# Optimization experiments

Hardware: AMD Instinct MI355X
Metric: run time of the kernel (lower is better)

Reference implementation:

```python
import jax, jax.numpy as jnp
import numpy as np

B, T, D = 2, 4096, 1024
H, L = 8, 2
DH = D // H           # 128
BS = 64               # bucket_size (lucidrains default)
NH = 8                # n_hashes (lucidrains default)
NB = T // BS          # 64 buckets (even, required)
FF = 4 * D


def setup_inputs() -> dict:
    key = jax.random.key(0)
    ks = jax.random.split(key, 16)
    s = 0.02
    return {
        'x': jax.random.normal(ks[0], (B, T, D), jnp.float32),
        'Wqk': jax.random.normal(ks[1], (L, D, H * DH), jnp.float32) * s,
        'Wv': jax.random.normal(ks[2], (L, D, H * DH), jnp.float32) * s,
        'Wout': jax.random.normal(ks[3], (L, H * DH, D), jnp.float32) * s,
        'bout': jnp.zeros((L, D), jnp.float32),
        'ln1_g': jnp.ones((L, D), jnp.float32),
        'ln1_b': jnp.zeros((L, D), jnp.float32),
        'W1': jax.random.normal(ks[4], (L, D, FF), jnp.float32) * s,
        'b1': jnp.zeros((L, FF), jnp.float32),
        'W2': jax.random.normal(ks[5], (L, FF, D), jnp.float32) * s,
        'b2': jnp.zeros((L, D), jnp.float32),
        'ln2_g': jnp.ones((L, D), jnp.float32),
        'ln2_b': jnp.zeros((L, D), jnp.float32),
        'rotations': jax.random.normal(ks[6], (L, DH, NH, NB // 2), jnp.float32),
    }


def _layer_norm(x, g, b):
    m = jnp.mean(x, axis=-1, keepdims=True)
    v = jnp.var(x, axis=-1, keepdims=True)
    return (x - m) * jax.lax.rsqrt(v + 1e-5) * g + b


def _look_one_back(x):
    # concat each chunk with the previous chunk (wrap-around), along the within-chunk axis
    return jnp.concatenate([x, jnp.roll(x, 1, axis=1)], axis=2)


def _lsh_attention(qk, v, rot):
    # qk, v: (bh, T, DH); rot: (DH, NH, NB//2). Causal LSH attention (lucidrains defaults).
    bh, t, d = qk.shape
    rotated = jnp.einsum('btd,dhr->bhtr', qk, rot)
    rotated = jnp.concatenate([rotated, -rotated], axis=-1)          # (bh, NH, T, NB)
    buckets = jnp.argmax(rotated, axis=-1)                            # (bh, NH, T)
    buckets = buckets + (jnp.arange(NH) * NB)[None, :, None]
    buckets = buckets.reshape(bh, NH * t)
    ticker = jnp.arange(NH * t)
    buckets_and_t = buckets * t + (ticker % t)
    sticker = jnp.argsort(buckets_and_t, axis=-1)                     # stable
    undo_sort = jnp.argsort(sticker, axis=-1)
    st = sticker % t                                                  # original positions
    sqk = jnp.take_along_axis(qk, st[..., None], axis=1)              # (bh, NH*T, DH)
    sv = jnp.take_along_axis(v, st[..., None], axis=1)
    n_chunks = NH * NB
    bq = sqk.reshape(bh, n_chunks, BS, d)
    norm = jnp.maximum(jnp.linalg.norm(sqk, axis=-1, keepdims=True), 1e-12)
    bk = (sqk / norm).reshape(bh, n_chunks, BS, d)
    bv = sv.reshape(bh, n_chunks, BS, d)
    bk = _look_one_back(bk)                                           # (bh, nc, 2*BS, d)
    bv = _look_one_back(bv)
    dots = jnp.einsum('bcie,bcje->bcij', bq, bk) * (d ** -0.5)
    bq_t = st.reshape(bh, n_chunks, BS)
    bkv_t = _look_one_back(bq_t[..., None] * jnp.ones((1,), st.dtype))[..., 0] if False else jnp.concatenate([bq_t, jnp.roll(bq_t, 1, axis=1)], axis=2)
    causal = bq_t[:, :, :, None] < bkv_t[:, :, None, :]
    dots = jnp.where(causal, -1e9, dots)
    self_mask = bq_t[:, :, :, None] == bkv_t[:, :, None, :]
    dots = jnp.where(self_mask, -5e4, dots)                           # TOKEN_SELF_ATTN_VALUE
    lse = jax.scipy.special.logsumexp(dots, axis=-1, keepdims=True)
    p = jnp.exp(dots - lse)
    bo = jnp.einsum('bcij,bcje->bcie', p, bv)
    so = bo.reshape(bh, NH * t, d)
    o = jnp.take_along_axis(so, undo_sort[..., None], axis=1)
    logits = jnp.take_along_axis(lse.reshape(bh, NH * t), undo_sort, axis=1)
    o = o.reshape(bh, NH, t, d)
    logits = logits.reshape(bh, NH, t, 1)
    probs = jnp.exp(logits - jax.scipy.special.logsumexp(logits, axis=1, keepdims=True))
    return jnp.sum(o * probs, axis=1)                                 # (bh, T, DH)


def _attn_block(x, Wqk, Wv, Wout, bout, g, b, rot):
    h = _layer_norm(x, g, b)
    qk = (h @ Wqk).reshape(B, T, H, DH).transpose(0, 2, 1, 3).reshape(B * H, T, DH)
    v = (h @ Wv).reshape(B, T, H, DH).transpose(0, 2, 1, 3).reshape(B * H, T, DH)
    o = _lsh_attention(qk, v, rot)
    o = o.reshape(B, H, T, DH).transpose(0, 2, 1, 3).reshape(B, T, H * DH)
    return o @ Wout + bout


def _ff_block(x, W1, b1, W2, b2, g, b):
    h = _layer_norm(x, g, b)
    return jax.nn.gelu(h @ W1 + b1, approximate=False) @ W2 + b2


def reference(x, Wqk, Wv, Wout, bout, ln1_g, ln1_b, W1, b1, W2, b2, ln2_g, ln2_b, rotations):
    # Reversible Reformer: x duplicated into two streams
    x1, x2 = x, x
    for l in range(L):
        x1 = x1 + _attn_block(x2, Wqk[l], Wv[l], Wout[l], bout[l], ln1_g[l], ln1_b[l], rotations[l])
        x2 = x2 + _ff_block(x1, W1[l], b1[l], W2[l], b2[l], ln2_g[l], ln2_b[l])
    out = (x1 + x2) * 0.5
    # mean-pool over sequence, reshape (1, B, D)
    return jnp.mean(out, axis=1).reshape(1, -1, D)
```

## Files before the change

### kernel.cpp

```cpp
#include <hip/hip_runtime.h>
#include <hip/hip_bf16.h>
#include <stdint.h>

#define B_ 2
#define T_ 4096
#define D_ 1024
#define H_ 8
#define DH_ 128
#define L_ 2
#define BS_ 64
#define NH_ 8
#define NB_ 64
#define NC_ (NH_*NB_)
#define FF_ 4096
#define BH_ (B_*H_)

typedef __hip_bfloat16 bf16;
typedef __attribute__((ext_vector_type(8))) short short8;
typedef __attribute__((ext_vector_type(4))) float f32x4;

typedef __attribute__((address_space(3))) uint32_t lds_u32_t;
typedef const __attribute__((address_space(1))) uint32_t glb_u32_t;

__device__ __forceinline__ void async_load16(const void* g, void* l) {
  __builtin_amdgcn_global_load_lds((glb_u32_t*)g, (lds_u32_t*)l, 16, 0, 0);
}

__global__ void diag_kernel(float* __restrict__ out, float a, float b) {
  if (threadIdx.x == 0) { out[0] = a; out[1] = b; }
}

__global__ void copy2_kernel(const float* __restrict__ x, float* __restrict__ x1,
                             float* __restrict__ x2) {
  int idx = blockIdx.x * 256 + threadIdx.x;
  if (idx < B_ * T_ * D_ / 4) {
    float4 v = ((const float4*)x)[idx];
    ((float4*)x1)[idx] = v;
    ((float4*)x2)[idx] = v;
  }
}

__global__ __launch_bounds__(256)
void transpose_cvt(const float* __restrict__ src, bf16* __restrict__ dst, int K, int N) {
  __shared__ float tile[32][33];
  const int n0 = blockIdx.x * 32, k0 = blockIdx.y * 32;
  const int c = threadIdx.x & 31, r8 = threadIdx.x >> 5;
#pragma unroll
  for (int i = 0; i < 32; i += 8) tile[r8 + i][c] = src[(size_t)(k0 + r8 + i) * N + n0 + c];
  __syncthreads();
#pragma unroll
  for (int i = 0; i < 32; i += 8)
    dst[(size_t)(n0 + r8 + i) * K + k0 + c] = __float2bfloat16(tile[c][r8 + i]);
}

__global__ __launch_bounds__(256)
void ln_kernel(const float* __restrict__ x, const float* __restrict__ g,
               const float* __restrict__ b, bf16* __restrict__ h) {
  __shared__ float red[8];
  const int row = blockIdx.x;
  const float* xr = x + (size_t)row * D_;
  const int tid = threadIdx.x;
  float4 xv = *(const float4*)(xr + tid * 4);
  float vals[4] = {xv.x, xv.y, xv.z, xv.w};
  float s = vals[0] + vals[1] + vals[2] + vals[3];
  float s2 = vals[0]*vals[0] + vals[1]*vals[1] + vals[2]*vals[2] + vals[3]*vals[3];
#pragma unroll
  for (int o = 1; o < 64; o <<= 1) { s += __shfl_xor(s, o, 64); s2 += __shfl_xor(s2, o, 64); }
  const int w = tid >> 6, lane = tid & 63;
  if (lane == 0) { red[w] = s; red[4 + w] = s2; }
  __syncthreads();
  s = red[0] + red[1] + red[2] + red[3];
  s2 = red[4] + red[5] + red[6] + red[7];
  const float mean = s * (1.0f / D_);
  const float var = s2 * (1.0f / D_) - mean * mean;
  const float rstd = rsqrtf(var + 1e-5f);
  bf16* hr = h + (size_t)row * D_;
#pragma unroll
  for (int i = 0; i < 4; ++i) {
    const int c = tid * 4 + i;
    hr[c] = __float2bfloat16((vals[i] - mean) * rstd * g[c] + b[c]);
  }
}

template<int EPI>
__global__ __launch_bounds__(512)
void gemm_bt_k(const bf16* __restrict__ A, const bf16* __restrict__ Bt,
               void* __restrict__ dst, const float* __restrict__ bias,
               float* __restrict__ resid, int M, int N, int K) {
  __shared__ __align__(16) bf16 sA[2][128 * 64];
  __shared__ __align__(16) bf16 sB[2][128 * 64];
  const int tid = threadIdx.x;

  const int GX = gridDim.x;
  const int nwg = GX * gridDim.y;
  const int orig = blockIdx.y * GX + blockIdx.x;
  int m0, n0;
  if ((nwg & 7) == 0 && (gridDim.y & 7) == 0) {
    const int cpx = nwg >> 3;
    const int lin = (orig & 7) * cpx + (orig >> 3);
    const int gsz = GX << 3;
    const int group = lin / gsz;
    const int rem = lin - group * gsz;
    m0 = ((group << 3) + (rem & 7)) << 7;
    n0 = (rem >> 3) << 7;
  } else {
    m0 = blockIdx.y << 7;
    n0 = blockIdx.x << 7;
  }

  const int lane = tid & 63;
  const int wv = tid >> 6;
  const int wm = (wv >> 2) << 6;
  const int wn = (wv & 3) << 5;
  const int l15 = lane & 15, lq = lane >> 4;

  f32x4 acc[4][2];
#pragma unroll
  for (int i = 0; i < 4; ++i)
#pragma unroll
    for (int j = 0; j < 2; ++j) acc[i][j] = (f32x4){0.f, 0.f, 0.f, 0.f};

  const bf16* Ab = A + (size_t)m0 * K;
  const bf16* Bb = Bt + (size_t)n0 * K;

  const int r0s = tid >> 3, ch0 = tid & 7;
  const int r1s = r0s + 64;
  const size_t sa0 = (size_t)r0s * K + (size_t)((ch0 ^ (r0s & 7)) << 3);
  const size_t sa1 = (size_t)r1s * K + (size_t)((ch0 ^ (r1s & 7)) << 3);

  auto stage = [&](int t) {
    const int b = t & 1;
    const size_t ko = (size_t)t << 6;
    async_load16(Ab + sa0 + ko, (char*)sA[b] + tid * 16);
    async_load16(Ab + sa1 + ko, (char*)sA[b] + (tid + 512) * 16);
    async_load16(Bb + sa0 + ko, (char*)sB[b] + tid * 16);
    async_load16(Bb + sa1 + ko, (char*)sB[b] + (tid + 512) * 16);
  };

  auto compute = [&](int b) {
    const bf16* __restrict__ pA = sA[b];
    const bf16* __restrict__ pB = sB[b];
#pragma unroll
    for (int kk = 0; kk < 2; ++kk) {
      short8 af[4], bfr[2];
#pragma unroll
      for (int mi = 0; mi < 4; ++mi) {
        const int row = wm + mi * 16 + l15;
        const int chunk = (kk * 4 + lq) ^ (row & 7);
        af[mi] = *(const short8*)(pA + (row << 6) + (chunk << 3));
      }
#pragma unroll
      for (int ni = 0; ni < 2; ++ni) {
        const int row = wn + ni * 16 + l15;
        const int chunk = (kk * 4 + lq) ^ (row & 7);
        bfr[ni] = *(const short8*)(pB + (row << 6) + (chunk << 3));
      }
#pragma unroll
      for (int mi = 0; mi < 4; ++mi)
#pragma unroll
        for (int ni = 0; ni < 2; ++ni)
          acc[mi][ni] = __builtin_amdgcn_mfma_f32_16x16x32_bf16(af[mi], bfr[ni], acc[mi][ni], 0, 0, 0);
    }
  };

  stage(0);
  __syncthreads();
  const int NT = K >> 6;
  for (int t = 0; t < NT; ++t) {
    if (t + 1 < NT) stage(t + 1);
    compute(t & 1);
    if (t + 1 < NT) __syncthreads();
  }

  const int cr = lq << 2;
  if (EPI == 5) {
    const int hh2 = (n0 + wn) >> 5;
#pragma unroll
    for (int mi = 0; mi < 4; ++mi) {
#pragma unroll
      for (int j = 0; j < 4; ++j) {
        const float v0 = acc[mi][0][j], v1 = acc[mi][1][j];
        float bmx = v0; int imx = l15;
        if (v1 > bmx) { bmx = v1; imx = 16 + l15; }
        float bmn = v0; int imn = l15;
        if (v1 < bmn) { bmn = v1; imn = 16 + l15; }
#pragma unroll
        for (int o = 1; o < 16; o <<= 1) {
          const float ov = __shfl_xor(bmx, o, 64); const int oi = __shfl_xor(imx, o, 64);
          if (ov > bmx || (ov == bmx && oi < imx)) { bmx = ov; imx = oi; }
          const float ov2 = __shfl_xor(bmn, o, 64); const int oi2 = __shfl_xor(imn, o, 64);
          if (ov2 < bmn || (ov2 == bmn && oi2 < imn)) { bmn = ov2; imn = oi2; }
        }
        if (l15 == 0) {
          const int r = m0 + wm + mi * 16 + cr + j;
          const int bh = r >> 12, t2 = r & (T_ - 1);
          const int bkt = (bmx >= -bmn) ? imx : 32 + imn;
          ((uint8_t*)dst)[((size_t)(bh * 8 + hh2) << 12) + t2] = (uint8_t)bkt;
        }
      }
    }
    return;
  }

#pragma unroll
  for (int mi = 0; mi < 4; ++mi) {
#pragma unroll
    for (int ni = 0; ni < 2; ++ni) {
#pragma unroll
      for (int j = 0; j < 4; ++j) {
        const int r = m0 + wm + mi * 16 + cr + j;
        const int c = n0 + wn + ni * 16 + l15;
        float val = acc[mi][ni][j];
        if (EPI == 0) {
          const int bb = r >> 12, t2 = r & (T_ - 1);
          const int hh = c >> 7, dh = c & (DH_ - 1);
          ((bf16*)dst)[(((size_t)(bb * H_ + hh)) * T_ + t2) * DH_ + dh] = __float2bfloat16(val);
        } else if (EPI == 2) {
          resid[(size_t)r * N + c] += val + bias[c];
        } else if (EPI == 3) {
          const float xg = val + bias[c];
          ((bf16*)dst)[(size_t)r * N + c] =
              __float2bfloat16(0.5f * xg * (1.0f + erff(xg * 0.70710678118654752440f)));
        } else if (EPI == 4) {
          ((bf16*)dst)[(size_t)r * N + c] = __float2bfloat16(val);
        }
      }
    }
  }
}

__global__ void bucket_kernel(const bf16* __restrict__ rotv, uint8_t* __restrict__ buckets) {
  const int idx = blockIdx.x * 256 + threadIdx.x;
  if (idx >= BH_ * T_ * NH_) return;
  const int row = idx >> 3, hh = idx & 7;
  const bf16* p = rotv + (size_t)row * 256 + hh * 32;
  float vmax = -3e38f, vmin = 3e38f;
  int imax = 0, imin = 0;
  for (int r = 0; r < 32; ++r) {
    const float xv = __bfloat162float(p[r]);
    if (xv > vmax) { vmax = xv; imax = r; }
    if (xv < vmin) { vmin = xv; imin = r; }
  }
  const int bkt = (vmax >= -vmin) ? imax : 32 + imin;
  const int bh = row >> 12, t = row & (T_ - 1);
  buckets[((size_t)(bh * 8 + hh) << 12) + t] = (uint8_t)bkt;
}

__global__ __launch_bounds__(256)
void sort_kernel(const uint8_t* __restrict__ buckets, int* __restrict__ st,
                 int* __restrict__ inv) {
  __shared__ uint8_t bk[T_];
  __shared__ int wsum[4];
  const int tid = threadIdx.x;
  const int grp = blockIdx.x;
  const uint8_t* src = buckets + (size_t)grp * T_;
  int* dst = st + (size_t)grp * T_;
  int* ivd = inv ? inv + (size_t)grp * T_ : nullptr;
  for (int i = tid; i < T_; i += 256) bk[i] = src[i];
  __syncthreads();
  const int lane = tid & 63, w = tid >> 6;
  const int t0 = tid * 16;
  int base = 0;
  for (int b = 0; b < 64; ++b) {
    int cnt = 0;
#pragma unroll
    for (int j = 0; j < 16; ++j) cnt += (bk[t0 + j] == b) ? 1 : 0;
    int incl = cnt;
    for (int o = 1; o < 64; o <<= 1) {
      int vv = __shfl_up(incl, o, 64);
      if (lane >= o) incl += vv;
    }
    if (lane == 63) wsum[w] = incl;
    __syncthreads();
    int wo = 0;
    for (int i = 0; i < w; ++i) wo += wsum[i];
    const int tot = wsum[0] + wsum[1] + wsum[2] + wsum[3];
    int pos = base + wo + incl - cnt;
    for (int j = 0; j < 16; ++j)
      if (bk[t0 + j] == b) {
        dst[pos] = t0 + j;
        if (ivd) ivd[t0 + j] = pos;
        ++pos;
      }
    base += tot;
    __syncthreads();
  }
}

__global__ __launch_bounds__(256)
void qknorm_kernel(const bf16* __restrict__ qk, bf16* __restrict__ qkn,
                   float* __restrict__ qnorm) {
  const int wid = (blockIdx.x * 256 + threadIdx.x) >> 6;
  const int lane = threadIdx.x & 63;
  if (wid >= BH_ * T_) return;
  const bf16* src = qk + (size_t)wid * DH_;
  const float a = __bfloat162float(src[2 * lane]);
  const float b = __bfloat162float(src[2 * lane + 1]);
  float ss = a * a + b * b;
#pragma unroll
  for (int o = 1; o < 64; o <<= 1) ss += __shfl_xor(ss, o, 64);
  const float nrm = sqrtf(ss);
  const float sc = 1.0f / fmaxf(nrm, 1e-12f);
  bf16* d = qkn + (size_t)wid * DH_;
  d[2 * lane] = __float2bfloat16(a * sc);
  d[2 * lane + 1] = __float2bfloat16(b * sc);
  if (lane == 0) qnorm[wid] = nrm;
}

__global__ __launch_bounds__(256)
void attn_sorted(const bf16* __restrict__ qkn, const float* __restrict__ qnormg,
                 const bf16* __restrict__ v, const int* __restrict__ st,
                 bf16* __restrict__ so, float* __restrict__ lseg) {
  __shared__ __align__(16) bf16 sK[128 * 136];
  __shared__ __align__(16) uint32_t sVT[128][68];
  __shared__ int stkv[128];
  __shared__ float snq[64];

  const int tid = threadIdx.x;
  const int lin = blockIdx.x;
  const int xcd = lin & 7;
  const int wq = lin >> 3;
  const int bh = xcd + ((wq >> 9) << 3);
  const int rem = wq & 511;
  const int hh = rem >> 6;
  const int cb = rem & 63;

  const int cg = hh * NB_ + cb;
  const int pg = (cg + NC_ - 1) & (NC_ - 1);
  const int* stb = st + (size_t)bh * (NH_ * T_);
  if (tid < 128) {
    const int p = (tid < 64) ? (cg * BS_ + tid) : (pg * BS_ + tid - 64);
    stkv[tid] = stb[p];
  }
  __syncthreads();

  const size_t vbase = (size_t)bh * T_ * DH_;
  if (tid < 64) snq[tid] = qnormg[(size_t)bh * T_ + stkv[tid]];
  {
    const int part = tid & 15, row = tid >> 4;
    for (int r0 = 0; r0 < 128; r0 += 16) {
      const int rr = r0 + row;
      const int t = stkv[rr];
      *(float4*)&sK[rr * 136 + part * 8] = *(const float4*)(qkn + vbase + (size_t)t * DH_ + part * 8);
    }
  }
  {
    for (int it = 0; it < 4; ++it) {
      const int idx = it * 256 + tid;
      const int g = idx & 15, kp = idx >> 4;
      const int t0 = stkv[2 * kp], t1 = stkv[2 * kp + 1];
      float4 a = *(const float4*)(v + vbase + (size_t)t0 * DH_ + g * 8);
      float4 b = *(const float4*)(v + vbase + (size_t)t1 * DH_ + g * 8);
      const unsigned short* ua = (const unsigned short*)&a;
      const unsigned short* ub = (const unsigned short*)&b;
      const int csw = (g & 7) << 2;
#pragma unroll
      for (int j = 0; j < 8; ++j)
        sVT[g * 8 + j][kp ^ csw] = (uint32_t)ua[j] | ((uint32_t)ub[j] << 16);
    }
  }
  __syncthreads();

  const int lane = tid & 63;
  const int w = tid >> 6;
  const int l15 = lane & 15, lq = lane >> 4;

  f32x4 acc[8];
#pragma unroll
  for (int i = 0; i < 8; ++i) acc[i] = (f32x4){0.f, 0.f, 0.f, 0.f};
#pragma unroll
  for (int kk = 0; kk < 4; ++kk) {
    short8 af = *(const short8*)&sK[(w * 16 + l15) * 136 + lq * 8 + kk * 32];
#pragma unroll
    for (int ni = 0; ni < 8; ++ni) {
      short8 bf = *(const short8*)&sK[(ni * 16 + l15) * 136 + lq * 8 + kk * 32];
      acc[ni] = __builtin_amdgcn_mfma_f32_16x16x32_bf16(af, bf, acc[ni], 0, 0, 0);
    }
  }
  __syncthreads();

  bf16* sP = sK;

  float lsev[4];
  const float scale = 0.08838834764831845f;
#pragma unroll
  for (int j = 0; j < 4; ++j) {
    const int row = w * 16 + lq * 4 + j;
    const int tq = stkv[row];
    const float rowsc = scale * snq[row];
    float mx = -3.0e38f;
#pragma unroll
    for (int ni = 0; ni < 8; ++ni) {
      const int tk = stkv[ni * 16 + l15];
      float val = acc[ni][j] * rowsc;
      if (tq < tk) val = -1e9f;
      else if (tq == tk) val = -5e4f;
      acc[ni][j] = val;
      mx = fmaxf(mx, val);
    }
#pragma unroll
    for (int o = 1; o < 16; o <<= 1) mx = fmaxf(mx, __shfl_xor(mx, o, 64));
    float se = 0.f;
#pragma unroll
    for (int ni = 0; ni < 8; ++ni) se += __expf(acc[ni][j] - mx);
#pragma unroll
    for (int o = 1; o < 16; o <<= 1) se += __shfl_xor(se, o, 64);
    const float inv = 1.0f / se;
#pragma unroll
    for (int ni = 0; ni < 8; ++ni)
      sP[row * 136 + ni * 16 + l15] = __float2bfloat16(__expf(acc[ni][j] - mx) * inv);
    lsev[j] = mx + __logf(se);
  }
  __syncthreads();

  f32x4 acc2[8];
#pragma unroll
  for (int i = 0; i < 8; ++i) acc2[i] = (f32x4){0.f, 0.f, 0.f, 0.f};
#pragma unroll
  for (int kk = 0; kk < 4; ++kk) {
    short8 pa = *(const short8*)&sP[(w * 16 + l15) * 136 + lq * 8 + kk * 32];
#pragma unroll
    for (int ni = 0; ni < 8; ++ni) {
      const int row = ni * 16 + l15;
      const int col = (lq * 4 + kk * 16) ^ (((row >> 3) & 7) << 2);
      short8 bv = *(const short8*)&sVT[row][col];
      acc2[ni] = __builtin_amdgcn_mfma_f32_16x16x32_bf16(pa, bv, acc2[ni], 0, 0, 0);
    }
  }

  const size_t sobase = ((size_t)(hh * BH_ + bh) * T_ + (size_t)cb * BS_) * DH_;
#pragma unroll
  for (int j = 0; j < 4; ++j) {
    const int row = w * 16 + lq * 4 + j;
    if (l15 == 0)
      lseg[(size_t)(hh * BH_ + bh) * T_ + cb * BS_ + row] = lsev[j];
    bf16* orow = so + sobase + (size_t)row * DH_;
#pragma unroll
    for (int ni = 0; ni < 8; ++ni) {
      bf16 hv = __float2bfloat16(acc2[ni][j]);
      __builtin_nontemporal_store(*(unsigned short*)&hv,
                                  (unsigned short*)(orow + ni * 16 + l15));
    }
  }
}

__global__ __launch_bounds__(256)
void combine2_kernel(const bf16* __restrict__ so, const float* __restrict__ lseg,
                     const int* __restrict__ ipos, bf16* __restrict__ ocomb) {
  const int gw = (blockIdx.x * 256 + threadIdx.x) >> 6;
  const int lane = threadIdx.x & 63;
  if (gw >= BH_ * T_) return;
  const int bh = gw >> 12, t = gw & (T_ - 1);
  float lse8 = -3.0e38f;
  int p8 = 0;
  if (lane < 8) {
    p8 = ipos[((size_t)bh * NH_ + lane) * T_ + t];
    lse8 = lseg[((size_t)lane * BH_ + bh) * T_ + p8];
  }
  float m = -3.0e38f;
#pragma unroll
  for (int h = 0; h < 8; ++h) m = fmaxf(m, __shfl(lse8, h, 64));
  float s = 0.f;
#pragma unroll
  for (int h = 0; h < 8; ++h) s += __expf(__shfl(lse8, h, 64) - m);
  const float invs = 1.0f / s;
  float a0 = 0.f, a1 = 0.f;
#pragma unroll
  for (int h = 0; h < 8; ++h) {
    const int ph = __shfl(p8, h, 64);
    const float wh = __expf(__shfl(lse8, h, 64) - m) * invs;
    const unsigned short* rp =
        (const unsigned short*)(so + (((size_t)h * BH_ + bh) * T_ + ph) * DH_ + lane * 2);
    unsigned short u0 = __builtin_nontemporal_load(rp);
    unsigned short u1 = __builtin_nontemporal_load(rp + 1);
    a0 += wh * __bfloat162float(*(const bf16*)&u0);
    a1 += wh * __bfloat162float(*(const bf16*)&u1);
  }
  const int bb = bh >> 3, hd = bh & 7;
  bf16* dp = ocomb + ((size_t)(bb * T_ + t)) * D_ + hd * DH_ + lane * 2;
  dp[0] = __float2bfloat16(a0);
  dp[1] = __float2bfloat16(a1);
}

__global__ __launch_bounds__(256)
void attn_kernel(const bf16* __restrict__ qkn, const float* __restrict__ qnormg,
                 const bf16* __restrict__ v, const int* __restrict__ st,
                 float* __restrict__ mg, float* __restrict__ sg,
                 float* __restrict__ oac, int hh) {
  __shared__ __align__(16) bf16 sK[128 * 136];
  __shared__ __align__(16) uint32_t sVT[128][68];
  __shared__ int stkv[128];
  __shared__ float snq[64];

  const int tid = threadIdx.x;
  const int cb = blockIdx.x;
  const int bh = blockIdx.y;
  const int cg = hh * NB_ + cb;
  const int pg = (cg + NC_ - 1) & (NC_ - 1);
  const int* stb = st + (size_t)bh * (NH_ * T_);
  if (tid < 128) {
    const int p = (tid < 64) ? (cg * BS_ + tid) : (pg * BS_ + tid - 64);
    stkv[tid] = stb[p];
  }
  __syncthreads();

  const size_t vbase = (size_t)bh * T_ * DH_;
  if (tid < 64) snq[tid] = qnormg[(size_t)bh * T_ + stkv[tid]];
  {
    const int part = tid & 15, row = tid >> 4;
    for (int r0 = 0; r0 < 128; r0 += 16) {
      const int rr = r0 + row;
      const int t = stkv[rr];
      *(float4*)&sK[rr * 136 + part * 8] = *(const float4*)(qkn + vbase + (size_t)t * DH_ + part * 8);
    }
  }
  {
    for (int it = 0; it < 4; ++it) {
      const int idx = it * 256 + tid;
      const int g = idx & 15, kp = idx >> 4;
      const int t0 = stkv[2 * kp], t1 = stkv[2 * kp + 1];
      float4 a = *(const float4*)(v + vbase + (size_t)t0 * DH_ + g * 8);
      float4 b = *(const float4*)(v + vbase + (size_t)t1 * DH_ + g * 8);
      const unsigned short* ua = (const unsigned short*)&a;
      const unsigned short* ub = (const unsigned short*)&b;
#pragma unroll
      for (int j = 0; j < 8; ++j)
        sVT[g * 8 + j][kp] = (uint32_t)ua[j] | ((uint32_t)ub[j] << 16);
    }
  }
  __syncthreads();

  const int lane = tid & 63;
  const int w = tid >> 6;
  const int l15 = lane & 15, lq = lane >> 4;

  f32x4 acc[8];
#pragma unroll
  for (int i = 0; i < 8; ++i) acc[i] = (f32x4){0.f, 0.f, 0.f, 0.f};
#pragma unroll
  for (int kk = 0; kk < 4; ++kk) {
    short8 af = *(const short8*)&sK[(w * 16 + l15) * 136 + lq * 8 + kk * 32];
#pragma unroll
    for (int ni = 0; ni < 8; ++ni) {
      short8 bf = *(const short8*)&sK[(ni * 16 + l15) * 136 + lq * 8 + kk * 32];
      acc[ni] = __builtin_amdgcn_mfma_f32_16x16x32_bf16(af, bf, acc[ni], 0, 0, 0);
    }
  }
  __syncthreads();

  bf16* sP = sK;

  float lsev[4];
  const float scale = 0.08838834764831845f;
#pragma unroll
  for (int j = 0; j < 4; ++j) {
    const int row = w * 16 + lq * 4 + j;
    const int tq = stkv[row];
    const float rowsc = scale * snq[row];
    float mx = -3.0e38f;
#pragma unroll
    for (int ni = 0; ni < 8; ++ni) {
      const int tk = stkv[ni * 16 + l15];
      float val = acc[ni][j] * rowsc;
      if (tq < tk) val = -1e9f;
      else if (tq == tk) val = -5e4f;
      acc[ni][j] = val;
      mx = fmaxf(mx, val);
    }
#pragma unroll
    for (int o = 1; o < 16; o <<= 1) mx = fmaxf(mx, __shfl_xor(mx, o, 64));
    float se = 0.f;
#pragma unroll
    for (int ni = 0; ni < 8; ++ni) se += __expf(acc[ni][j] - mx);
#pragma unroll
    for (int o = 1; o < 16; o <<= 1) se += __shfl_xor(se, o, 64);
    const float inv = 1.0f / se;
#pragma unroll
    for (int ni = 0; ni < 8; ++ni)
      sP[row * 136 + ni * 16 + l15] = __float2bfloat16(__expf(acc[ni][j] - mx) * inv);
    lsev[j] = mx + __logf(se);
  }
  __syncthreads();

  f32x4 acc2[8];
#pragma unroll
  for (int i = 0; i < 8; ++i) acc2[i] = (f32x4){0.f, 0.f, 0.f, 0.f};
#pragma unroll
  for (int kk = 0; kk < 4; ++kk) {
    short8 pa = *(const short8*)&sP[(w * 16 + l15) * 136 + lq * 8 + kk * 32];
#pragma unroll
    for (int ni = 0; ni < 8; ++ni) {
      short8 bv = *(const short8*)&sVT[ni * 16 + l15][lq * 4 + kk * 16];
      acc2[ni] = __builtin_amdgcn_mfma_f32_16x16x32_bf16(pa, bv, acc2[ni], 0, 0, 0);
    }
  }

#pragma unroll
  for (int j = 0; j < 4; ++j) {
    const int row = w * 16 + lq * 4 + j;
    const int t = stkv[row];
    const size_t gi = (size_t)bh * T_ + t;
    const float ls = lsev[j];
    float* orow = oac + gi * DH_;
    if (hh == 0) {
      if (l15 == 0) { sg[gi] = 1.0f; mg[gi] = ls; }
#pragma unroll
      for (int ni = 0; ni < 8; ++ni) orow[ni * 16 + l15] = acc2[ni][j];
    } else {
      const float mo = mg[gi];
      const float mn = fmaxf(mo, ls);
      const float al = __expf(mo - mn);
      const float be = __expf(ls - mn);
      if (l15 == 0) { sg[gi] = sg[gi] * al + be; mg[gi] = mn; }
#pragma unroll
      for (int ni = 0; ni < 8; ++ni) {
        const int c = ni * 16 + l15;
        orow[c] = orow[c] * al + be * acc2[ni][j];
      }
    }
  }
}

__global__ void combine_kernel(const float* __restrict__ oac, const float* __restrict__ sg,
                               bf16* __restrict__ ocomb) {
  const int idx = blockIdx.x * 256 + threadIdx.x;
  if (idx >= BH_ * T_ * DH_ / 4) return;
  const int rowtok = idx >> 5;
  const int gsub = idx & 31;
  const float inv = 1.0f / sg[rowtok];
  float4 ov = ((const float4*)oac)[idx];
  const int bh = rowtok >> 12, t = rowtok & (T_ - 1);
  const int bb = bh >> 3, hd = bh & 7;
  bf16* dp = ocomb + ((size_t)(bb * T_ + t)) * D_ + hd * DH_ + gsub * 4;
  dp[0] = __float2bfloat16(ov.x * inv);
  dp[1] = __float2bfloat16(ov.y * inv);
  dp[2] = __float2bfloat16(ov.z * inv);
  dp[3] = __float2bfloat16(ov.w * inv);
}

__global__ void pool_partial(const float* __restrict__ x1, const float* __restrict__ x2,
                             float* __restrict__ part) {
  const int b = blockIdx.y, slice = blockIdx.x;
  const int tid = threadIdx.x;
  float acc[4] = {0.f, 0.f, 0.f, 0.f};
  for (int r = 0; r < 32; ++r) {
    const size_t base = ((size_t)b * T_ + slice * 32 + r) * D_;
#pragma unroll
    for (int i = 0; i < 4; ++i) {
      const int c = tid + i * 256;
      acc[i] += x1[base + c] + x2[base + c];
    }
  }
#pragma unroll
  for (int i = 0; i < 4; ++i)
    part[((size_t)(b * 128 + slice)) * D_ + tid + i * 256] = acc[i];
}

__global__ void pool_reduce(const float* __restrict__ part, float* __restrict__ out) {
  const int idx = blockIdx.x * 256 + threadIdx.x;
  if (idx >= B_ * D_) return;
  const int b = idx >> 10, d = idx & 1023;
  float s = 0.f;
  for (int k = 0; k < 128; ++k) s += part[((size_t)(b * 128 + k)) * D_ + d];
  out[idx] = s * (0.5f / T_);
}

extern "C" void kernel_launch(void* const* d_in, const int* in_sizes, int n_in,
                              void* d_out, int out_size, void* d_ws, size_t ws_size,
                              hipStream_t stream) {
  (void)in_sizes; (void)n_in; (void)out_size;
  const float* x    = (const float*)d_in[0];
  const float* Wqk  = (const float*)d_in[1];
  const float* Wv   = (const float*)d_in[2];
  const float* Wout = (const float*)d_in[3];
  const float* bout = (const float*)d_in[4];
  const float* ln1g = (const float*)d_in[5];
  const float* ln1b = (const float*)d_in[6];
  const float* W1   = (const float*)d_in[7];
  const float* b1   = (const float*)d_in[8];
  const float* W2   = (const float*)d_in[9];
  const float* b2   = (const float*)d_in[10];
  const float* ln2g = (const float*)d_in[11];
  const float* ln2b = (const float*)d_in[12];
  const float* rot  = (const float*)d_in[13];
  float* out = (float*)d_out;

  char* ws = (char*)d_ws;
  const dim3 blk(256);
  const dim3 blk512(512);

  {
    size_t off = 0;
    auto alloc = [&](size_t b) { size_t o = off; off += (b + 255) & ~(size_t)255; return o; };
    const size_t o_x1  = alloc((size_t)B_ * T_ * D_ * 4);
    const size_t o_x2  = alloc((size_t)B_ * T_ * D_ * 4);
    const size_t o_hq  = alloc((size_t)B_ * T_ * D_ * 2);
    const size_t o_qk  = alloc((size_t)BH_ * T_ * DH_ * 2);
    const size_t o_vv  = alloc((size_t)BH_ * T_ * DH_ * 2);
    const size_t o_so  = alloc((size_t)NH_ * BH_ * T_ * DH_ * 2);
    const size_t o_lse = alloc((size_t)NH_ * BH_ * T_ * 4);
    const size_t o_st  = alloc((size_t)BH_ * NH_ * T_ * 4);
    const size_t o_ip  = alloc((size_t)BH_ * NH_ * T_ * 4);
    const size_t o_bkt = alloc((size_t)BH_ * NH_ * T_);
    const size_t o_qn  = alloc((size_t)BH_ * T_ * 4);
    const size_t o_part = alloc((size_t)B_ * 128 * D_ * 4);

    if (off <= ws_size) {
      float* x1   = (float*)(ws + o_x1);
      float* x2   = (float*)(ws + o_x2);
      bf16*  h    = (bf16*)(ws + o_hq);
      bf16*  qkn  = (bf16*)(ws + o_hq);
      bf16*  qk   = (bf16*)(ws + o_qk);
      bf16*  ocomb = (bf16*)(ws + o_qk);
      bf16*  vv   = (bf16*)(ws + o_vv);
      bf16*  so   = (bf16*)(ws + o_so);
      float* lse  = (float*)(ws + o_lse);
      int*   st   = (int*)(ws + o_st);
      int*   ip   = (int*)(ws + o_ip);
      uint8_t* bkt = (uint8_t*)(ws + o_bkt);
      float* qn   = (float*)(ws + o_qn);
      float* part = (float*)(ws + o_part);
      bf16* wqkT = (bf16*)(ws + o_so);
      bf16* wvT  = wqkT + (size_t)D_ * D_;
      bf16* rotT = wvT + (size_t)D_ * D_;
      bf16* woT  = (bf16*)(ws + o_so);
      bf16* ffh  = (bf16*)(ws + o_so);
      bf16* w1T  = (bf16*)(ws + o_so + ((size_t)64 << 20));
      bf16* w2T  = w1T + (size_t)D_ * FF_;

      copy2_kernel<<<dim3(B_ * T_ * D_ / 4 / 256), blk, 0, stream>>>(x, x1, x2);

      for (int l = 0; l < L_; ++l) {
        transpose_cvt<<<dim3(32, 32), blk, 0, stream>>>(Wqk + (size_t)l * D_ * D_, wqkT, D_, D_);
        transpose_cvt<<<dim3(32, 32), blk, 0, stream>>>(Wv + (size_t)l * D_ * D_, wvT, D_, D_);
        transpose_cvt<<<dim3(8, 4), blk, 0, stream>>>(rot + (size_t)l * DH_ * 256, rotT, DH_, 256);

        ln_kernel<<<dim3(B_ * T_), blk, 0, stream>>>(x2, ln1g + l * D_, ln1b + l * D_, h);
        gemm_bt_k<0><<<dim3(8, 64), blk512, 0, stream>>>(h, wqkT, qk, nullptr, nullptr, B_ * T_, D_, D_);
        gemm_bt_k<0><<<dim3(8, 64), blk512, 0, stream>>>(h, wvT, vv, nullptr, nullptr, B_ * T_, D_, D_);
        qknorm_kernel<<<dim3(BH_ * T_ / 4), blk, 0, stream>>>(qk, qkn, qn);
        gemm_bt_k<5><<<dim3(2, 512), blk512, 0, stream>>>(qkn, rotT, bkt, nullptr, nullptr, BH_ * T_, 256, DH_);
        sort_kernel<<<dim3(BH_ * NH_), blk, 0, stream>>>(bkt, st, ip);
        attn_sorted<<<dim3(NB_ * BH_ * NH_), blk, 0, stream>>>(qkn, qn, vv, st, so, lse);
        combine2_kernel<<<dim3(BH_ * T_ / 4), blk, 0, stream>>>(so, lse, ip, ocomb);
        transpose_cvt<<<dim3(32, 32), blk, 0, stream>>>(Wout + (size_t)l * D_ * D_, woT, D_, D_);
        gemm_bt_k<2><<<dim3(8, 64), blk512, 0, stream>>>(ocomb, woT, nullptr, bout + l * D_, x1, B_ * T_, D_, D_);

        transpose_cvt<<<dim3(128, 32), blk, 0, stream>>>(W1 + (size_t)l * D_ * FF_, w1T, D_, FF_);
        transpose_cvt<<<dim3(32, 128), blk, 0, stream>>>(W2 + (size_t)l * FF_ * D_, w2T, FF_, D_);
        ln_kernel<<<dim3(B_ * T_), blk, 0, stream>>>(x1, ln2g + l * D_, ln2b + l * D_, h);
        gemm_bt_k<3><<<dim3(32, 64), blk512, 0, stream>>>(h, w1T, ffh, b1 + l * FF_, nullptr, B_ * T_, FF_, D_);
        gemm_bt_k<2><<<dim3(8, 64), blk512, 0, stream>>>(ffh, w2T, nullptr, b2 + l * D_, x2, B_ * T_, D_, FF_);
      }

      pool_partial<<<dim3(128, B_), blk, 0, stream>>>(x1, x2, part);
      pool_reduce<<<dim3((B_ * D_ + 255) / 256), blk, 0, stream>>>(part, out);
      return;
    }
  }

  size_t off = 0;
  auto alloc = [&](size_t b) { size_t o = off; off += (b + 255) & ~(size_t)255; return o; };
  const size_t o_x1   = alloc((size_t)B_ * T_ * D_ * 4);
  const size_t o_x2   = alloc((size_t)B_ * T_ * D_ * 4);
  const size_t o_hq   = alloc((size_t)B_ * T_ * D_ * 2);
  const size_t o_qk   = alloc((size_t)BH_ * T_ * DH_ * 2);
  const size_t o_vv   = alloc((size_t)BH_ * T_ * DH_ * 2);
  const size_t o_oac  = alloc((size_t)BH_ * T_ * DH_ * 4);
  const size_t o_st   = alloc((size_t)BH_ * NH_ * T_ * 4);
  const size_t o_bkt  = alloc((size_t)BH_ * NH_ * T_);
  const size_t o_mg   = alloc((size_t)BH_ * T_ * 4);
  const size_t o_sg   = alloc((size_t)BH_ * T_ * 4);
  const size_t o_qn   = alloc((size_t)BH_ * T_ * 4);
  const size_t o_part = alloc((size_t)B_ * 128 * D_ * 4);
  const size_t o_w    = alloc((size_t)D_ * FF_ * 2 * 2);
  if (off > ws_size) {
    diag_kernel<<<dim3(1), dim3(64), 0, stream>>>(out, (float)ws_size, (float)off);
    return;
  }

  float* x1   = (float*)(ws + o_x1);
  float* x2   = (float*)(ws + o_x2);
  bf16*  h    = (bf16*)(ws + o_hq);
  bf16*  qkn  = (bf16*)(ws + o_hq);
  bf16*  qk   = (bf16*)(ws + o_qk);
  bf16*  ocomb = (bf16*)(ws + o_qk);
  bf16*  vv   = (bf16*)(ws + o_vv);
  float* oac  = (float*)(ws + o_oac);
  bf16*  rotd = (bf16*)(ws + o_oac);
  bf16*  ffh  = (bf16*)(ws + o_qk);
  int*   st   = (int*)(ws + o_st);
  uint8_t* bkt = (uint8_t*)(ws + o_bkt);
  float* mg   = (float*)(ws + o_mg);
  float* sg   = (float*)(ws + o_sg);
  float* qn   = (float*)(ws + o_qn);
  float* part = (float*)(ws + o_part);
  bf16* wqkT = (bf16*)(ws + o_w);
  bf16* wvT  = (bf16*)(ws + o_w + (size_t)D_ * D_ * 2);
  bf16* woT  = (bf16*)(ws + o_w + (size_t)D_ * D_ * 2 * 2);
  bf16* rotT = (bf16*)(ws + o_w + (size_t)D_ * D_ * 2 * 3);
  bf16* w1T  = (bf16*)(ws + o_w);
  bf16* w2T  = (bf16*)(ws + o_w + (size_t)D_ * FF_ * 2);

  copy2_kernel<<<dim3(B_ * T_ * D_ / 4 / 256), blk, 0, stream>>>(x, x1, x2);

  for (int l = 0; l < L_; ++l) {
    transpose_cvt<<<dim3(32, 32), blk, 0, stream>>>(Wqk + (size_t)l * D_ * D_, wqkT, D_, D_);
    transpose_cvt<<<dim3(32, 32), blk, 0, stream>>>(Wv + (size_t)l * D_ * D_, wvT, D_, D_);
    transpose_cvt<<<dim3(32, 32), blk, 0, stream>>>(Wout + (size_t)l * D_ * D_, woT, D_, D_);
    transpose_cvt<<<dim3(8, 4), blk, 0, stream>>>(rot + (size_t)l * DH_ * 256, rotT, DH_, 256);

    ln_kernel<<<dim3(B_ * T_), blk, 0, stream>>>(x2, ln1g + l * D_, ln1b + l * D_, h);
    gemm_bt_k<0><<<dim3(8, 64), blk512, 0, stream>>>(h, wqkT, qk, nullptr, nullptr, B_ * T_, D_, D_);
    gemm_bt_k<0><<<dim3(8, 64), blk512, 0, stream>>>(h, wvT, vv, nullptr, nullptr, B_ * T_, D_, D_);
    qknorm_kernel<<<dim3(BH_ * T_ / 4), blk, 0, stream>>>(qk, qkn, qn);
    gemm_bt_k<4><<<dim3(2, 512), blk512, 0, stream>>>(qkn, rotT, rotd, nullptr, nullptr, BH_ * T_, 256, DH_);
    bucket_kernel<<<dim3(BH_ * T_ * NH_ / 256), blk, 0, stream>>>(rotd, bkt);
    sort_kernel<<<dim3(BH_ * NH_), blk, 0, stream>>>(bkt, st, nullptr);
    for (int hh = 0; hh < NH_; ++hh)
      attn_kernel<<<dim3(NB_, BH_), blk, 0, stream>>>(qkn, qn, vv, st, mg, sg, oac, hh);
    combine_kernel<<<dim3(BH_ * T_ * DH_ / 4 / 256), blk, 0, stream>>>(oac, sg, ocomb);
    gemm_bt_k<2><<<dim3(8, 64), blk512, 0, stream>>>(ocomb, woT, nullptr, bout + l * D_, x1, B_ * T_, D_, D_);

    transpose_cvt<<<dim3(128, 32), blk, 0, stream>>>(W1 + (size_t)l * D_ * FF_, w1T, D_, FF_);
    transpose_cvt<<<dim3(32, 128), blk, 0, stream>>>(W2 + (size_t)l * FF_ * D_, w2T, FF_, D_);

    ln_kernel<<<dim3(B_ * T_), blk, 0, stream>>>(x1, ln2g + l * D_, ln2b + l * D_, h);
    gemm_bt_k<3><<<dim3(32, 64), blk512, 0, stream>>>(h, w1T, ffh, b1 + l * FF_, nullptr, B_ * T_, FF_, D_);
    gemm_bt_k<2><<<dim3(8, 64), blk512, 0, stream>>>(ffh, w2T, nullptr, b2 + l * D_, x2, B_ * T_, D_, FF_);
  }

  pool_partial<<<dim3(128, B_), blk, 0, stream>>>(x1, x2, part);
  pool_reduce<<<dim3((B_ * D_ + 255) / 256), blk, 0, stream>>>(part, out);
}
```

Measured before the change: 1.154 ms.

## Add 256x256-tile GEMM, fuse QK and V projections, cache softmax exps

Adds a 256x256 output-tile GEMM kernel with double-buffered LDS staging and MFMA bf16. It runs the fused QK+V projection as one N=2048 GEMM that relies on wqkT and wvT being contiguous, and the FF1 GEMM with GELU. The larger tile raises arithmetic intensity and cuts the launch count. The cost is 128KB of LDS per block and many accumulator registers, which limits occupancy. The attention softmax also keeps the exp values instead of computing them twice.

```diff
diff --git a/kernel.cpp b/kernel.cpp
--- a/kernel.cpp
+++ b/kernel.cpp
@@ -79,6 +79,130 @@
   for (int i = 0; i < 4; ++i) {
     const int c = tid * 4 + i;
     hr[c] = __float2bfloat16((vals[i] - mean) * rstd * g[c] + b[c]);
+  }
+}
+
+template<int EPI>
+__global__ __launch_bounds__(512)
+void gemm256(const bf16* __restrict__ A, const bf16* __restrict__ Bt,
+             void* __restrict__ dst, const float* __restrict__ bias,
+             float* __restrict__ resid, int M, int N, int K) {
+  __shared__ __align__(16) bf16 sA[2][256 * 64];
+  __shared__ __align__(16) bf16 sB[2][256 * 64];
+  const int tid = threadIdx.x;
+
+  const int GX = gridDim.x;
+  const int nwg = GX * gridDim.y;
+  const int orig = blockIdx.y * GX + blockIdx.x;
+  int m0, n0;
+  if ((nwg & 7) == 0 && (gridDim.y & 7) == 0) {
+    const int cpx = nwg >> 3;
+    const int lin = (orig & 7) * cpx + (orig >> 3);
+    const int gsz = GX << 3;
+    const int group = lin / gsz;
+    const int rem = lin - group * gsz;
+    m0 = ((group << 3) + (rem & 7)) << 8;
+    n0 = (rem >> 3) << 8;
+  } else {
+    m0 = blockIdx.y << 8;
+    n0 = blockIdx.x << 8;
+  }
+
+  const int lane = tid & 63;
+  const int wv = tid >> 6;
+  const int wm = (wv >> 2) << 7;
+  const int wn = (wv & 3) << 6;
+  const int l15 = lane & 15, lq = lane >> 4;
+
+  f32x4 acc[8][4];
+#pragma unroll
+  for (int i = 0; i < 8; ++i)
+#pragma unroll
+    for (int j = 0; j < 4; ++j) acc[i][j] = (f32x4){0.f, 0.f, 0.f, 0.f};
+
+  const bf16* Ab = A + (size_t)m0 * K;
+  const bf16* Bb = Bt + (size_t)n0 * K;
+  const int ch0 = tid & 7;
+
+  auto stage_pass = [&](int buf, int t, int p) {
+    const size_t ko = (size_t)t << 6;
+    const int r = (tid >> 3) + (p << 6);
+    const size_t ga = (size_t)r * K + (size_t)((ch0 ^ (r & 7)) << 3) + ko;
+    async_load16(Ab + ga, (char*)sA[buf] + (p << 13) + tid * 16);
+    async_load16(Bb + ga, (char*)sB[buf] + (p << 13) + tid * 16);
+  };
+
+#pragma unroll
+  for (int p = 0; p < 4; ++p) stage_pass(0, 0, p);
+  __syncthreads();
+
+  const int NT = K >> 6;
+  short8 bfr[4][2];
+  for (int t = 0; t < NT; ++t) {
+    const int cur = t & 1;
+    const bf16* __restrict__ pA = sA[cur];
+    const bf16* __restrict__ pB = sB[cur];
+#pragma unroll
+    for (int p = 0; p < 4; ++p) {
+      if (t + 1 < NT) stage_pass(cur ^ 1, t + 1, p);
+      if (p == 0) {
+#pragma unroll
+        for (int ni = 0; ni < 4; ++ni)
+#pragma unroll
+          for (int kk = 0; kk < 2; ++kk) {
+            const int row = wn + ni * 16 + l15;
+            bfr[ni][kk] = *(const short8*)(pB + (row << 6) + (((kk * 4 + lq) ^ (row & 7)) << 3));
+          }
+      }
+      short8 af[2][2];
+#pragma unroll
+      for (int m2 = 0; m2 < 2; ++m2)
+#pragma unroll
+        for (int kk = 0; kk < 2; ++kk) {
+          const int row = wm + (2 * p + m2) * 16 + l15;
+          af[m2][kk] = *(const short8*)(pA + (row << 6) + (((kk * 4 + lq) ^ (row & 7)) << 3));
+        }
+      __builtin_amdgcn_s_setprio(1);
+#pragma unroll
+      for (int m2 = 0; m2 < 2; ++m2)
+#pragma unroll
+        for (int ni = 0; ni < 4; ++ni)
+#pragma unroll
+          for (int kk = 0; kk < 2; ++kk)
+            acc[2 * p + m2][ni] =
+                __builtin_amdgcn_mfma_f32_16x16x32_bf16(af[m2][kk], bfr[ni][kk], acc[2 * p + m2][ni], 0, 0, 0);
+      __builtin_amdgcn_s_setprio(0);
+    }
+    if (t + 1 < NT) __syncthreads();
+  }
+
+  const int cr = lq << 2;
+#pragma unroll
+  for (int mi = 0; mi < 8; ++mi) {
+#pragma unroll
+    for (int ni = 0; ni < 4; ++ni) {
+#pragma unroll
+      for (int j = 0; j < 4; ++j) {
+        const int r = m0 + wm + mi * 16 + cr + j;
+        const int c = n0 + wn + ni * 16 + l15;
+        const float val = acc[mi][ni][j];
+        if (EPI == 0) {
+          const int bb = r >> 12, t2 = r & (T_ - 1);
+          if (c < 1024) {
+            const int hh = c >> 7, dh = c & (DH_ - 1);
+            ((bf16*)dst)[(((size_t)(bb * H_ + hh)) * T_ + t2) * DH_ + dh] = __float2bfloat16(val);
+          } else {
+            const int c2 = c - 1024;
+            const int hh = c2 >> 7, dh = c2 & (DH_ - 1);
+            ((bf16*)resid)[(((size_t)(bb * H_ + hh)) * T_ + t2) * DH_ + dh] = __float2bfloat16(val);
+          }
+        } else if (EPI == 3) {
+          const float xg = val + bias[c];
+          ((bf16*)dst)[(size_t)r * N + c] =
+              __float2bfloat16(0.5f * xg * (1.0f + erff(xg * 0.70710678118654752440f)));
+        }
+      }
+    }
   }
 }
 
@@ -400,15 +524,16 @@
     }
 #pragma unroll
     for (int o = 1; o < 16; o <<= 1) mx = fmaxf(mx, __shfl_xor(mx, o, 64));
+    float ex[8];
     float se = 0.f;
 #pragma unroll
-    for (int ni = 0; ni < 8; ++ni) se += __expf(acc[ni][j] - mx);
+    for (int ni = 0; ni < 8; ++ni) { ex[ni] = __expf(acc[ni][j] - mx); se += ex[ni]; }
 #pragma unroll
     for (int o = 1; o < 16; o <<= 1) se += __shfl_xor(se, o, 64);
     const float inv = 1.0f / se;
 #pragma unroll
     for (int ni = 0; ni < 8; ++ni)
-      sP[row * 136 + ni * 16 + l15] = __float2bfloat16(__expf(acc[ni][j] - mx) * inv);
+      sP[row * 136 + ni * 16 + l15] = __float2bfloat16(ex[ni] * inv);
     lsev[j] = mx + __logf(se);
   }
   __syncthreads();
@@ -736,8 +861,8 @@
         transpose_cvt<<<dim3(8, 4), blk, 0, stream>>>(rot + (size_t)l * DH_ * 256, rotT, DH_, 256);
 
         ln_kernel<<<dim3(B_ * T_), blk, 0, stream>>>(x2, ln1g + l * D_, ln1b + l * D_, h);
-        gemm_bt_k<0><<<dim3(8, 64), blk512, 0, stream>>>(h, wqkT, qk, nullptr, nullptr, B_ * T_, D_, D_);
-        gemm_bt_k<0><<<dim3(8, 64), blk512, 0, stream>>>(h, wvT, vv, nullptr, nullptr, B_ * T_, D_, D_);
+        gemm256<0><<<dim3(8, 32), blk512, 0, stream>>>(h, wqkT, qk, nullptr, (float*)vv,
+                                                       B_ * T_, 2048, D_);
         qknorm_kernel<<<dim3(BH_ * T_ / 4), blk, 0, stream>>>(qk, qkn, qn);
         gemm_bt_k<5><<<dim3(2, 512), blk512, 0, stream>>>(qkn, rotT, bkt, nullptr, nullptr, BH_ * T_, 256, DH_);
         sort_kernel<<<dim3(BH_ * NH_), blk, 0, stream>>>(bkt, st, ip);
@@ -749,7 +874,8 @@
         transpose_cvt<<<dim3(128, 32), blk, 0, stream>>>(W1 + (size_t)l * D_ * FF_, w1T, D_, FF_);
         transpose_cvt<<<dim3(32, 128), blk, 0, stream>>>(W2 + (size_t)l * FF_ * D_, w2T, FF_, D_);
         ln_kernel<<<dim3(B_ * T_), blk, 0, stream>>>(x1, ln2g + l * D_, ln2b + l * D_, h);
-        gemm_bt_k<3><<<dim3(32, 64), blk512, 0, stream>>>(h, w1T, ffh, b1 + l * FF_, nullptr, B_ * T_, FF_, D_);
+        gemm256<3><<<dim3(16, 32), blk512, 0, stream>>>(h, w1T, ffh, b1 + l * FF_,
+                                                        nullptr, B_ * T_, FF_, D_);
         gemm_bt_k<2><<<dim3(8, 64), blk512, 0, stream>>>(ffh, w2T, nullptr, b2 + l * D_, x2, B_ * T_, D_, FF_);
       }
 
```

New measurement: 1.196 ms. 3.7% more time.

## Fuse QK and V projections into one GEMM and alias V tile into score LDS

Applied to the files above, without the earlier changes.

The QK and V projection GEMMs become a single launch with N=2048. This relies on wvT sitting directly after wqkT in memory, and the new epilogue routes columns to either the qk or the v head-major buffer. In the attention kernel, V rows are loaded into registers early, then transposed into LDS after the softmax. The upper half of the transposed V is placed in the now-free part of the score buffer, which cuts LDS use and may raise occupancy, at the cost of more live registers.

```diff
diff --git a/kernel.cpp b/kernel.cpp
--- a/kernel.cpp
+++ b/kernel.cpp
@@ -223,6 +223,16 @@
               __float2bfloat16(0.5f * xg * (1.0f + erff(xg * 0.70710678118654752440f)));
         } else if (EPI == 4) {
           ((bf16*)dst)[(size_t)r * N + c] = __float2bfloat16(val);
+        } else if (EPI == 6) {
+          const int bb = r >> 12, t2 = r & (T_ - 1);
+          if (c < 1024) {
+            const int hh = c >> 7, dh = c & (DH_ - 1);
+            ((bf16*)dst)[(((size_t)(bb * H_ + hh)) * T_ + t2) * DH_ + dh] = __float2bfloat16(val);
+          } else {
+            const int c2 = c - 1024;
+            const int hh = c2 >> 7, dh = c2 & (DH_ - 1);
+            ((bf16*)resid)[(((size_t)(bb * H_ + hh)) * T_ + t2) * DH_ + dh] = __float2bfloat16(val);
+          }
         }
       }
     }
@@ -312,7 +322,7 @@
                  const bf16* __restrict__ v, const int* __restrict__ st,
                  bf16* __restrict__ so, float* __restrict__ lseg) {
   __shared__ __align__(16) bf16 sK[128 * 136];
-  __shared__ __align__(16) uint32_t sVT[128][68];
+  __shared__ __align__(16) uint32_t sVTlo[64 * 68];
   __shared__ int stkv[128];
   __shared__ float snq[64];
 
@@ -344,20 +354,13 @@
       *(float4*)&sK[rr * 136 + part * 8] = *(const float4*)(qkn + vbase + (size_t)t * DH_ + part * 8);
     }
   }
-  {
-    for (int it = 0; it < 4; ++it) {
-      const int idx = it * 256 + tid;
-      const int g = idx & 15, kp = idx >> 4;
-      const int t0 = stkv[2 * kp], t1 = stkv[2 * kp + 1];
-      float4 a = *(const float4*)(v + vbase + (size_t)t0 * DH_ + g * 8);
-      float4 b = *(const float4*)(v + vbase + (size_t)t1 * DH_ + g * 8);
-      const unsigned short* ua = (const unsigned short*)&a;
-      const unsigned short* ub = (const unsigned short*)&b;
-      const int csw = (g & 7) << 2;
-#pragma unroll
-      for (int j = 0; j < 8; ++j)
-        sVT[g * 8 + j][kp ^ csw] = (uint32_t)ua[j] | ((uint32_t)ub[j] << 16);
-    }
+  float4 va[4], vb[4];
+#pragma unroll
+  for (int it = 0; it < 4; ++it) {
+    const int idx = it * 256 + tid;
+    const int g = idx & 15, kp = idx >> 4;
+    va[it] = *(const float4*)(v + vbase + (size_t)stkv[2 * kp] * DH_ + g * 8);
+    vb[it] = *(const float4*)(v + vbase + (size_t)stkv[2 * kp + 1] * DH_ + g * 8);
   }
   __syncthreads();
 
@@ -380,6 +383,7 @@
   __syncthreads();
 
   bf16* sP = sK;
+  uint32_t* sVThi = (uint32_t*)(sK + 64 * 136);
 
   float lsev[4];
   const float scale = 0.08838834764831845f;
@@ -400,16 +404,30 @@
     }
 #pragma unroll
     for (int o = 1; o < 16; o <<= 1) mx = fmaxf(mx, __shfl_xor(mx, o, 64));
+    float ex[8];
     float se = 0.f;
 #pragma unroll
-    for (int ni = 0; ni < 8; ++ni) se += __expf(acc[ni][j] - mx);
+    for (int ni = 0; ni < 8; ++ni) { ex[ni] = __expf(acc[ni][j] - mx); se += ex[ni]; }
 #pragma unroll
     for (int o = 1; o < 16; o <<= 1) se += __shfl_xor(se, o, 64);
     const float inv = 1.0f / se;
 #pragma unroll
     for (int ni = 0; ni < 8; ++ni)
-      sP[row * 136 + ni * 16 + l15] = __float2bfloat16(__expf(acc[ni][j] - mx) * inv);
+      sP[row * 136 + ni * 16 + l15] = __float2bfloat16(ex[ni] * inv);
     lsev[j] = mx + __logf(se);
+  }
+
+#pragma unroll
+  for (int it = 0; it < 4; ++it) {
+    const int idx = it * 256 + tid;
+    const int g = idx & 15, kp = idx >> 4;
+    const unsigned short* ua = (const unsigned short*)&va[it];
+    const unsigned short* ub = (const unsigned short*)&vb[it];
+    const int csw = (g & 7) << 2;
+    uint32_t* vdst = (g < 8) ? (sVTlo + g * 8 * 68) : (sVThi + (g - 8) * 8 * 68);
+#pragma unroll
+    for (int j = 0; j < 8; ++j)
+      vdst[j * 68 + (kp ^ csw)] = (uint32_t)ua[j] | ((uint32_t)ub[j] << 16);
   }
   __syncthreads();
 
@@ -423,7 +441,8 @@
     for (int ni = 0; ni < 8; ++ni) {
       const int row = ni * 16 + l15;
       const int col = (lq * 4 + kk * 16) ^ (((row >> 3) & 7) << 2);
-      short8 bv = *(const short8*)&sVT[row][col];
+      const uint32_t* vrow = (ni < 4) ? (sVTlo + row * 68) : (sVThi + (row - 64) * 68);
+      short8 bv = *(const short8*)&vrow[col];
       acc2[ni] = __builtin_amdgcn_mfma_f32_16x16x32_bf16(pa, bv, acc2[ni], 0, 0, 0);
     }
   }
@@ -736,8 +755,8 @@
         transpose_cvt<<<dim3(8, 4), blk, 0, stream>>>(rot + (size_t)l * DH_ * 256, rotT, DH_, 256);
 
         ln_kernel<<<dim3(B_ * T_), blk, 0, stream>>>(x2, ln1g + l * D_, ln1b + l * D_, h);
-        gemm_bt_k<0><<<dim3(8, 64), blk512, 0, stream>>>(h, wqkT, qk, nullptr, nullptr, B_ * T_, D_, D_);
-        gemm_bt_k<0><<<dim3(8, 64), blk512, 0, stream>>>(h, wvT, vv, nullptr, nullptr, B_ * T_, D_, D_);
+        gemm_bt_k<6><<<dim3(16, 64), blk512, 0, stream>>>(h, wqkT, qk, nullptr, (float*)vv,
+                                                          B_ * T_, 2048, D_);
         qknorm_kernel<<<dim3(BH_ * T_ / 4), blk, 0, stream>>>(qk, qkn, qn);
         gemm_bt_k<5><<<dim3(2, 512), blk512, 0, stream>>>(qkn, rotT, bkt, nullptr, nullptr, BH_ * T_, 256, DH_);
         sort_kernel<<<dim3(BH_ * NH_), blk, 0, stream>>>(bkt, st, ip);
```

New measurement: 1.104 ms. 1.04x faster.
